# Kernel optimization log

Hardware: AMD Instinct MI355X
Metric: run time of the kernel (lower is better)

Reference implementation:

```python
import jax, jax.numpy as jnp
import numpy as np

N_NODES = 100000


def gcn_conv(x, W, b, src, dst, ew, n):
    """PyG GCNConv with edge_weight: add self-loops (weight 1), symmetric norm,
    linear transform, scatter-add aggregation, bias."""
    h = x @ W                                   # [N, F_out]
    # degree includes the self-loop weight of 1 per node
    deg = jnp.zeros((n,), dtype=x.dtype).at[dst].add(ew) + 1.0
    dinv = jax.lax.rsqrt(deg)                   # deg > 0 always (self-loop)
    norm = dinv[src] * ew * dinv[dst]           # [E]
    agg = jax.ops.segment_sum(h[src] * norm[:, None], dst, num_segments=n)
    # self-loop contribution: norm_ii = dinv[i]^2 * 1
    agg = agg + h * (dinv * dinv)[:, None]
    return agg + b


def setup_inputs() -> dict:
    key = jax.random.key(0)
    ks = jax.random.split(key, 9)
    N, E, F_in, F_h, F_out = N_NODES, 1600000, 128, 64, 10
    x = jax.random.normal(ks[0], (N, F_in), dtype=jnp.float32)
    edge_index = jax.random.randint(ks[1], (2, E), 0, N, dtype=jnp.int64)
    edge_weight = jax.random.uniform(ks[2], (E,), dtype=jnp.float32)
    def glorot(k, fi, fo):
        s = jnp.sqrt(6.0 / (fi + fo))
        return jax.random.uniform(k, (fi, fo), minval=-s, maxval=s, dtype=jnp.float32)
    return {
        "x": x,
        "edge_index": edge_index,
        "edge_weight": edge_weight,
        "W1": glorot(ks[3], F_in, F_h), "b1": jnp.zeros((F_h,), jnp.float32),
        "W2": glorot(ks[4], F_h, F_h), "b2": jnp.zeros((F_h,), jnp.float32),
        "Wfc": glorot(ks[5], F_h, F_out), "bfc": jnp.zeros((F_out,), jnp.float32),
    }


def reference(x, edge_index, edge_weight, W1, b1, W2, b2, Wfc, bfc):
    n = x.shape[0]
    src, dst = edge_index[0], edge_index[1]
    h = gcn_conv(x, W1, b1, src, dst, edge_weight, n)
    h = jax.nn.relu(h)
    h = gcn_conv(h, W2, b2, src, dst, edge_weight, n)
    h = jax.nn.relu(h)
    return h @ Wfc + bfc
```

## Files before the change

kernel.cpp:

```cpp
#include <hip/hip_runtime.h>

static constexpr int F_IN  = 128;
static constexpr int F_H   = 64;
static constexpr int F_OUT = 10;

static constexpr int NPB_SHIFT = 9;
static constexpr int NPB = 1 << NPB_SHIFT;
static constexpr int MAXC = 256;
static constexpr int EPB = 4096;

__device__ __forceinline__ unsigned short f2bf(float f) {
    unsigned u = __float_as_uint(f);
    return (unsigned short)((u + 0x7fff + ((u >> 16) & 1)) >> 16);
}
__device__ __forceinline__ float bf_lo(unsigned u) { return __uint_as_float(u << 16); }
__device__ __forceinline__ float bf_hi(unsigned u) { return __uint_as_float(u & 0xffff0000u); }

__device__ __forceinline__ int load_idx(const void* ein, bool f64, long i) {
    return f64 ? (int)((const long long*)ein)[i] : ((const int*)ein)[i];
}

__global__ __launch_bounds__(256) void k_part1(const void* __restrict__ ein,
                                               const float* __restrict__ ew,
                                               int* __restrict__ gcur,
                                               unsigned long long* __restrict__ packed,
                                               int E, int NC, int cap) {
    __shared__ int lcnt[MAXC];
    __shared__ int lofs[MAXC];
    __shared__ int sflag;
    int tid = threadIdx.x;
    if (tid < NC) lcnt[tid] = 0;
    if (tid < 64) {
        unsigned long long v = ((const unsigned long long*)ein)[tid];
        int hz = ((v >> 32) == 0ull) ? 1 : 0;
        int all64 = __all(hz);
        if (tid == 0) sflag = all64;
    }
    __syncthreads();
    bool f = sflag != 0;
    int base = blockIdx.x * EPB;
    int   es[16];
    int   ed[16];
    float ww[16];
#pragma unroll
    for (int j = 0; j < 16; ++j) {
        int e = base + j * 256 + tid;
        if (e < E) {
            es[j] = load_idx(ein, f, e);
            ed[j] = load_idx(ein, f, (long)E + e);
            ww[j] = ew[e];
            atomicAdd(&lcnt[ed[j] >> NPB_SHIFT], 1);
        }
    }
    __syncthreads();
    if (tid < NC) {
        int c = lcnt[tid];
        lofs[tid] = c ? atomicAdd(&gcur[tid], c) : 0;
        lcnt[tid] = 0;
    }
    __syncthreads();
#pragma unroll
    for (int j = 0; j < 16; ++j) {
        int e = base + j * 256 + tid;
        if (e < E) {
            int b = ed[j] >> NPB_SHIFT;
            int pos = lofs[b] + atomicAdd(&lcnt[b], 1);
            if (pos < cap) {
                unsigned long long u = (unsigned long long)__float_as_uint(ww[j])
                                     | ((unsigned long long)(unsigned)es[j] << 32)
                                     | ((unsigned long long)(unsigned)(ed[j] & (NPB - 1)) << 49);
                packed[(long)b * cap + pos] = u;
            }
        }
    }
}

__global__ __launch_bounds__(256) void k_chist(const unsigned long long* __restrict__ packed,
                                               const int* __restrict__ gcur,
                                               int* __restrict__ rp,
                                               int* __restrict__ pbt,
                                               float* __restrict__ dinv,
                                               int N, int cap) {
    __shared__ int   lc[NPB];
    __shared__ float ld[NPB];
    __shared__ int   sm[256];
    int b = blockIdx.x, tid = threadIdx.x;
#pragma unroll
    for (int i = tid; i < NPB; i += 256) { lc[i] = 0; ld[i] = 0.0f; }
    __syncthreads();
    int cnt = gcur[b];
    const unsigned long long* pk = packed + (long)b * cap;
    for (int p = tid; p < cnt; p += 256) {
        unsigned long long u = pk[p];
        int dl = (int)(u >> 49);
        atomicAdd(&lc[dl], 1);
        atomicAdd(&ld[dl], __uint_as_float((unsigned int)u));
    }
    __syncthreads();
    int c0 = lc[tid * 2], c1 = lc[tid * 2 + 1];
    int pp0 = (c0 + 15) & ~15, pp1 = (c1 + 15) & ~15;
    int s = pp0 + pp1;
    sm[tid] = s;
    __syncthreads();
    for (int off = 1; off < 256; off <<= 1) {
        int v = 0;
        if (tid >= off) v = sm[tid - off];
        __syncthreads();
        sm[tid] += v;
        __syncthreads();
    }
    int excl = sm[tid] - s;
    int n0 = b << NPB_SHIFT;
    int node0 = n0 + tid * 2, node1 = node0 + 1;
    if (node0 < N) {
        rp[node0]   = excl;
        dinv[node0] = rsqrtf(ld[tid * 2] + 1.0f);
    }
    if (node1 < N) {
        rp[node1]   = excl + pp0;
        dinv[node1] = rsqrtf(ld[tid * 2 + 1] + 1.0f);
    }
    if (tid == 255) pbt[b] = sm[255];
}

__global__ __launch_bounds__(256) void k_cscatter(const unsigned long long* __restrict__ packed,
                                                  const int* __restrict__ gcur,
                                                  const int* __restrict__ rp,
                                                  const int* __restrict__ pbt,
                                                  const float* __restrict__ dinv,
                                                  uint2* __restrict__ recs,
                                                  int* __restrict__ rpabs,
                                                  int N, int NC, int cap) {
    __shared__ int   cur[NPB];
    __shared__ float dd[NPB];
    __shared__ int   sm[256];
    int b = blockIdx.x, tid = threadIdx.x;
    int c = (tid < NC) ? pbt[tid] : 0;
    sm[tid] = c;
    __syncthreads();
    for (int off = 1; off < 256; off <<= 1) {
        int v = 0;
        if (tid >= off) v = sm[tid - off];
        __syncthreads();
        sm[tid] += v;
        __syncthreads();
    }
    int pbtb = pbt[b];
    int pb_  = sm[b] - pbtb;
    if (b == NC - 1 && tid == 255) rpabs[N] = sm[255];
    int n0 = b << NPB_SHIFT;
#pragma unroll
    for (int i = tid; i < NPB; i += 256) {
        int node = n0 + i;
        int r = (node < N) ? rp[node] + pb_ : 0;
        cur[i] = r;
        dd[i]  = (node < N) ? dinv[node] : 0.0f;
        if (node < N) rpabs[node] = r;
    }
    __syncthreads();
    int cnt = gcur[b];
    const unsigned long long* pk = packed + (long)b * cap;
    for (int p = tid; p < cnt; p += 256) {
        unsigned long long u = pk[p];
        int dl = (int)(u >> 49);
        int s  = (int)((u >> 32) & 0x1FFFF);
        float w = __uint_as_float((unsigned int)u);
        int pos = atomicAdd(&cur[dl], 1);
        uint2 r;
        r.x = (unsigned)(s << 7);
        r.y = __float_as_uint(dinv[s] * w * dd[dl]);
        recs[pos] = r;
    }
    __syncthreads();
    for (int i = tid; i < NPB; i += 256) {
        int node = n0 + i;
        if (node < N) {
            int el = (i == NPB - 1 || node + 1 >= N) ? pbtb : rp[node + 1];
            int end = el + pb_;
            for (int p = cur[i]; p < end; ++p) recs[p] = make_uint2(0u, 0u);
        }
    }
}

template <int K, bool ABF16>
__global__ __launch_bounds__(256) void k_gemm(const void* __restrict__ A,
                                              const float* __restrict__ W,
                                              unsigned short* __restrict__ Cb, int M) {
    __shared__ float As[128][32];
    __shared__ float Ws[32][64];
    int tid = threadIdx.x;
    int tx = tid & 15;
    int ty = tid >> 4;
    int rb = blockIdx.x * 128;
    float acc[8][4] = {};
    for (int kc = 0; kc < K; kc += 32) {
        __syncthreads();
#pragma unroll
        for (int i = 0; i < 4; ++i) {
            int e = tid + i * 256;
            int r = e >> 3, g = e & 7;
            int gr = rb + r;
            float4 v = make_float4(0.f, 0.f, 0.f, 0.f);
            if (gr < M) {
                if (ABF16) {
                    uint2 u = *(const uint2*)&((const unsigned short*)A)[(long)gr * K + kc + g * 4];
                    v = make_float4(bf_lo(u.x), bf_hi(u.x), bf_lo(u.y), bf_hi(u.y));
                } else {
                    v = *(const float4*)&((const float*)A)[(long)gr * K + kc + g * 4];
                }
            }
            int gs = g ^ ((r >> 3) & 7);
            *(float4*)&As[r][gs * 4] = v;
        }
#pragma unroll
        for (int i = 0; i < 2; ++i) {
            int e = tid + i * 256;
            int k = e >> 4, n4 = e & 15;
            *(float4*)&Ws[k][n4 * 4] = *(const float4*)&W[(long)(kc + k) * 64 + n4 * 4];
        }
        __syncthreads();
#pragma unroll
        for (int g = 0; g < 8; ++g) {
            float4 b0 = *(const float4*)&Ws[g * 4 + 0][tx * 4];
            float4 b1 = *(const float4*)&Ws[g * 4 + 1][tx * 4];
            float4 b2 = *(const float4*)&Ws[g * 4 + 2][tx * 4];
            float4 b3 = *(const float4*)&Ws[g * 4 + 3][tx * 4];
            int gs = (g ^ (ty & 7)) * 4;
#pragma unroll
            for (int rr = 0; rr < 8; ++rr) {
                float4 a = *(const float4*)&As[ty * 8 + rr][gs];
                acc[rr][0] = fmaf(a.x, b0.x, acc[rr][0]);
                acc[rr][1] = fmaf(a.x, b0.y, acc[rr][1]);
                acc[rr][2] = fmaf(a.x, b0.z, acc[rr][2]);
                acc[rr][3] = fmaf(a.x, b0.w, acc[rr][3]);
                acc[rr][0] = fmaf(a.y, b1.x, acc[rr][0]);
                acc[rr][1] = fmaf(a.y, b1.y, acc[rr][1]);
                acc[rr][2] = fmaf(a.y, b1.z, acc[rr][2]);
                acc[rr][3] = fmaf(a.y, b1.w, acc[rr][3]);
                acc[rr][0] = fmaf(a.z, b2.x, acc[rr][0]);
                acc[rr][1] = fmaf(a.z, b2.y, acc[rr][1]);
                acc[rr][2] = fmaf(a.z, b2.z, acc[rr][2]);
                acc[rr][3] = fmaf(a.z, b2.w, acc[rr][3]);
                acc[rr][0] = fmaf(a.w, b3.x, acc[rr][0]);
                acc[rr][1] = fmaf(a.w, b3.y, acc[rr][1]);
                acc[rr][2] = fmaf(a.w, b3.z, acc[rr][2]);
                acc[rr][3] = fmaf(a.w, b3.w, acc[rr][3]);
            }
        }
    }
#pragma unroll
    for (int rr = 0; rr < 8; ++rr) {
        int gr = rb + ty * 8 + rr;
        if (gr < M) {
            ushort4 v;
            v.x = f2bf(acc[rr][0]); v.y = f2bf(acc[rr][1]);
            v.z = f2bf(acc[rr][2]); v.w = f2bf(acc[rr][3]);
            *(ushort4*)&Cb[(long)gr * 64 + tx * 4] = v;
        }
    }
}

__global__ __launch_bounds__(256, 4) void k_agg(const unsigned short* __restrict__ hb,
                                                const int* __restrict__ rp,
                                                const uint2* __restrict__ recs,
                                                const float* __restrict__ dinv,
                                                const float* __restrict__ bias,
                                                unsigned short* __restrict__ outb, int N) {
    int wid  = (blockIdx.x * 256 + threadIdx.x) >> 6;
    int lane = threadIdx.x & 63;
    int fg   = lane & 15;
    int es   = lane >> 4;
    if (wid >= N) return;
    int fg8 = fg * 8;
    const char* hbase = (const char*)hb;
    int p0 = rp[wid], p1 = rp[wid + 1];
    float a0 = 0.f, a1 = 0.f, a2 = 0.f, a3 = 0.f;
    int pb = p0 + es * 4;
    for (; pb + 16 < p1; pb += 32) {
        uint4 r01 = *(const uint4*)&recs[pb];
        uint4 r23 = *(const uint4*)&recs[pb + 2];
        uint4 r45 = *(const uint4*)&recs[pb + 16];
        uint4 r67 = *(const uint4*)&recs[pb + 18];
        uint2 h0 = *(const uint2*)(hbase + r01.x + fg8);
        uint2 h1 = *(const uint2*)(hbase + r01.z + fg8);
        uint2 h2 = *(const uint2*)(hbase + r23.x + fg8);
        uint2 h3 = *(const uint2*)(hbase + r23.z + fg8);
        uint2 h4 = *(const uint2*)(hbase + r45.x + fg8);
        uint2 h5 = *(const uint2*)(hbase + r45.z + fg8);
        uint2 h6 = *(const uint2*)(hbase + r67.x + fg8);
        uint2 h7 = *(const uint2*)(hbase + r67.z + fg8);
        float w0 = __uint_as_float(r01.y), w1 = __uint_as_float(r01.w);
        float w2 = __uint_as_float(r23.y), w3 = __uint_as_float(r23.w);
        float w4 = __uint_as_float(r45.y), w5 = __uint_as_float(r45.w);
        float w6 = __uint_as_float(r67.y), w7 = __uint_as_float(r67.w);
        a0 = fmaf(w0, bf_lo(h0.x), a0); a1 = fmaf(w0, bf_hi(h0.x), a1);
        a2 = fmaf(w0, bf_lo(h0.y), a2); a3 = fmaf(w0, bf_hi(h0.y), a3);
        a0 = fmaf(w1, bf_lo(h1.x), a0); a1 = fmaf(w1, bf_hi(h1.x), a1);
        a2 = fmaf(w1, bf_lo(h1.y), a2); a3 = fmaf(w1, bf_hi(h1.y), a3);
        a0 = fmaf(w2, bf_lo(h2.x), a0); a1 = fmaf(w2, bf_hi(h2.x), a1);
        a2 = fmaf(w2, bf_lo(h2.y), a2); a3 = fmaf(w2, bf_hi(h2.y), a3);
        a0 = fmaf(w3, bf_lo(h3.x), a0); a1 = fmaf(w3, bf_hi(h3.x), a1);
        a2 = fmaf(w3, bf_lo(h3.y), a2); a3 = fmaf(w3, bf_hi(h3.y), a3);
        a0 = fmaf(w4, bf_lo(h4.x), a0); a1 = fmaf(w4, bf_hi(h4.x), a1);
        a2 = fmaf(w4, bf_lo(h4.y), a2); a3 = fmaf(w4, bf_hi(h4.y), a3);
        a0 = fmaf(w5, bf_lo(h5.x), a0); a1 = fmaf(w5, bf_hi(h5.x), a1);
        a2 = fmaf(w5, bf_lo(h5.y), a2); a3 = fmaf(w5, bf_hi(h5.y), a3);
        a0 = fmaf(w6, bf_lo(h6.x), a0); a1 = fmaf(w6, bf_hi(h6.x), a1);
        a2 = fmaf(w6, bf_lo(h6.y), a2); a3 = fmaf(w6, bf_hi(h6.y), a3);
        a0 = fmaf(w7, bf_lo(h7.x), a0); a1 = fmaf(w7, bf_hi(h7.x), a1);
        a2 = fmaf(w7, bf_lo(h7.y), a2); a3 = fmaf(w7, bf_hi(h7.y), a3);
    }
    if (pb < p1) {
        uint4 r01 = *(const uint4*)&recs[pb];
        uint4 r23 = *(const uint4*)&recs[pb + 2];
        uint2 h0 = *(const uint2*)(hbase + r01.x + fg8);
        uint2 h1 = *(const uint2*)(hbase + r01.z + fg8);
        uint2 h2 = *(const uint2*)(hbase + r23.x + fg8);
        uint2 h3 = *(const uint2*)(hbase + r23.z + fg8);
        float w0 = __uint_as_float(r01.y), w1 = __uint_as_float(r01.w);
        float w2 = __uint_as_float(r23.y), w3 = __uint_as_float(r23.w);
        a0 = fmaf(w0, bf_lo(h0.x), a0); a1 = fmaf(w0, bf_hi(h0.x), a1);
        a2 = fmaf(w0, bf_lo(h0.y), a2); a3 = fmaf(w0, bf_hi(h0.y), a3);
        a0 = fmaf(w1, bf_lo(h1.x), a0); a1 = fmaf(w1, bf_hi(h1.x), a1);
        a2 = fmaf(w1, bf_lo(h1.y), a2); a3 = fmaf(w1, bf_hi(h1.y), a3);
        a0 = fmaf(w2, bf_lo(h2.x), a0); a1 = fmaf(w2, bf_hi(h2.x), a1);
        a2 = fmaf(w2, bf_lo(h2.y), a2); a3 = fmaf(w2, bf_hi(h2.y), a3);
        a0 = fmaf(w3, bf_lo(h3.x), a0); a1 = fmaf(w3, bf_hi(h3.x), a1);
        a2 = fmaf(w3, bf_lo(h3.y), a2); a3 = fmaf(w3, bf_hi(h3.y), a3);
    }
#pragma unroll
    for (int m = 16; m <= 32; m <<= 1) {
        a0 += __shfl_xor(a0, m);
        a1 += __shfl_xor(a1, m);
        a2 += __shfl_xor(a2, m);
        a3 += __shfl_xor(a3, m);
    }
    float di  = dinv[wid];
    float di2 = di * di;
    uint2 hs = *(const uint2*)(hbase + ((long)wid << 7) + fg8);
    float4 bv = *(const float4*)&bias[fg * 4];
    a0 = fmaf(bf_lo(hs.x), di2, a0 + bv.x);
    a1 = fmaf(bf_hi(hs.x), di2, a1 + bv.y);
    a2 = fmaf(bf_lo(hs.y), di2, a2 + bv.z);
    a3 = fmaf(bf_hi(hs.y), di2, a3 + bv.w);
    if (es == 0) {
        ushort4 r;
        r.x = f2bf(fmaxf(a0, 0.f));
        r.y = f2bf(fmaxf(a1, 0.f));
        r.z = f2bf(fmaxf(a2, 0.f));
        r.w = f2bf(fmaxf(a3, 0.f));
        *(ushort4*)&outb[(long)wid * 64 + fg * 4] = r;
    }
}

__global__ __launch_bounds__(256) void k_fc(const unsigned short* __restrict__ hb,
                                            const float* __restrict__ W,
                                            const float* __restrict__ b,
                                            float* __restrict__ out, int N) {
    __shared__ float Ws[64 * 10];
    __shared__ float bs[16];
    int tid = threadIdx.x;
    for (int e = tid; e < 64 * 10; e += 256) Ws[e] = W[e];
    if (tid < 10) bs[tid] = b[tid];
    __syncthreads();
    int i = blockIdx.x * 256 + tid;
    if (i >= N) return;
    float acc[10];
#pragma unroll
    for (int j = 0; j < 10; ++j) acc[j] = bs[j];
    const uint2* row = (const uint2*)&hb[(long)i * 64];
#pragma unroll
    for (int c = 0; c < 16; ++c) {
        uint2 u = row[c];
        float ax = bf_lo(u.x), ay = bf_hi(u.x);
        float az = bf_lo(u.y), aw = bf_hi(u.y);
#pragma unroll
        for (int j = 0; j < 10; ++j) {
            acc[j] = fmaf(ax, Ws[(4 * c + 0) * 10 + j], acc[j]);
            acc[j] = fmaf(ay, Ws[(4 * c + 1) * 10 + j], acc[j]);
            acc[j] = fmaf(az, Ws[(4 * c + 2) * 10 + j], acc[j]);
            acc[j] = fmaf(aw, Ws[(4 * c + 3) * 10 + j], acc[j]);
        }
    }
#pragma unroll
    for (int j = 0; j < 10; ++j) out[(long)i * 10 + j] = acc[j];
}

extern "C" void kernel_launch(void* const* d_in, const int* in_sizes, int n_in,
                              void* d_out, int out_size, void* d_ws, size_t ws_size,
                              hipStream_t stream) {
    const float* x    = (const float*)d_in[0];
    const void*  eidx = d_in[1];
    const float* ew   = (const float*)d_in[2];
    const float* W1   = (const float*)d_in[3];
    const float* b1   = (const float*)d_in[4];
    const float* W2   = (const float*)d_in[5];
    const float* b2   = (const float*)d_in[6];
    const float* Wfc  = (const float*)d_in[7];
    const float* bfc  = (const float*)d_in[8];
    float* out = (float*)d_out;

    const int N  = in_sizes[0] / F_IN;
    const int E  = in_sizes[2];
    const int NC = (N + NPB - 1) >> NPB_SHIFT;
    const int cap = E / NC + E / (8 * NC) + 1024;

    char* w = (char*)d_ws;
    size_t off = 0;
    auto alloc = [&](size_t bytes) {
        void* p = w + off;
        off += (bytes + 255) & ~(size_t)255;
        return p;
    };
    float* dinv  = (float*)alloc((size_t)N * 4);
    int*   rp    = (int*)alloc((size_t)(N + 1) * 4);
    int*   rpabs = (int*)alloc((size_t)(N + 1) * 4);
    int*   gcur  = (int*)alloc((size_t)MAXC * 4);
    int*   pbt   = (int*)alloc((size_t)MAXC * 4);
    unsigned long long* packed =
        (unsigned long long*)alloc((size_t)NC * cap * 8);
    uint2* recs  = (uint2*)alloc(((size_t)E + 15u * (size_t)N + 64) * 8);
    unsigned short* h1b = (unsigned short*)alloc((size_t)N * F_H * 2);
    unsigned short* g1b = (unsigned short*)alloc((size_t)N * F_H * 2);
    unsigned short* h2b = h1b;
    unsigned short* g2b = g1b;
    (void)ws_size;

    hipMemsetAsync(gcur, 0, (size_t)NC * 4, stream);

    const int PB = (E + EPB - 1) / EPB;

    k_part1<<<PB, 256, 0, stream>>>(eidx, ew, gcur, packed, E, NC, cap);
    k_chist<<<NC, 256, 0, stream>>>(packed, gcur, rp, pbt, dinv, N, cap);
    k_cscatter<<<NC, 256, 0, stream>>>(packed, gcur, rp, pbt, dinv, recs,
                                       rpabs, N, NC, cap);

    const int GB = (N + 127) / 128;
    k_gemm<F_IN, false><<<GB, 256, 0, stream>>>(x, W1, h1b, N);
    k_agg<<<(N + 3) / 4, 256, 0, stream>>>(h1b, rpabs, recs, dinv, b1, g1b, N);
    k_gemm<F_H, true><<<GB, 256, 0, stream>>>(g1b, W2, h2b, N);
    k_agg<<<(N + 3) / 4, 256, 0, stream>>>(h2b, rpabs, recs, dinv, b2, g2b, N);
    k_fc<<<(N + 255) / 256, 256, 0, stream>>>(g2b, Wfc, bfc, out, N);
}
```

Measured before the change: 203.7 us.

## Merge edge partitioning and first-layer GEMM into one heterogeneous launch

The edge bucketing kernel and the first x@W1 GEMM are combined into a single launch. Blocks below PB do the edge partitioning and the remaining blocks compute the bf16 h1 tiles, so the two independent phases can share the GPU at the same time and one launch is removed. The cost is higher shared memory per block, since the GEMM tiles are always allocated, which may lower occupancy for the partition blocks.

Result: faster. 194.7 us (-4.4%).

```diff
diff --git a/kernel.cpp b/kernel.cpp
--- a/kernel.cpp
+++ b/kernel.cpp
@@ -20,56 +20,127 @@
     return f64 ? (int)((const long long*)ein)[i] : ((const int*)ein)[i];
 }
 
-__global__ __launch_bounds__(256) void k_part1(const void* __restrict__ ein,
-                                               const float* __restrict__ ew,
-                                               int* __restrict__ gcur,
-                                               unsigned long long* __restrict__ packed,
-                                               int E, int NC, int cap) {
+__global__ __launch_bounds__(256) void k_pre(const void* __restrict__ ein,
+                                             const float* __restrict__ ew,
+                                             int* __restrict__ gcur,
+                                             unsigned long long* __restrict__ packed,
+                                             int E, int NC, int cap, int PB,
+                                             const float* __restrict__ x,
+                                             const float* __restrict__ W1,
+                                             unsigned short* __restrict__ h1b, int M) {
     __shared__ int lcnt[MAXC];
     __shared__ int lofs[MAXC];
     __shared__ int sflag;
+    __shared__ float As[128][32];
+    __shared__ float Ws[32][64];
     int tid = threadIdx.x;
-    if (tid < NC) lcnt[tid] = 0;
-    if (tid < 64) {
-        unsigned long long v = ((const unsigned long long*)ein)[tid];
-        int hz = ((v >> 32) == 0ull) ? 1 : 0;
-        int all64 = __all(hz);
-        if (tid == 0) sflag = all64;
-    }
-    __syncthreads();
-    bool f = sflag != 0;
-    int base = blockIdx.x * EPB;
-    int   es[16];
-    int   ed[16];
-    float ww[16];
-#pragma unroll
-    for (int j = 0; j < 16; ++j) {
-        int e = base + j * 256 + tid;
-        if (e < E) {
-            es[j] = load_idx(ein, f, e);
-            ed[j] = load_idx(ein, f, (long)E + e);
-            ww[j] = ew[e];
-            atomicAdd(&lcnt[ed[j] >> NPB_SHIFT], 1);
-        }
-    }
-    __syncthreads();
-    if (tid < NC) {
-        int c = lcnt[tid];
-        lofs[tid] = c ? atomicAdd(&gcur[tid], c) : 0;
-        lcnt[tid] = 0;
-    }
-    __syncthreads();
-#pragma unroll
-    for (int j = 0; j < 16; ++j) {
-        int e = base + j * 256 + tid;
-        if (e < E) {
-            int b = ed[j] >> NPB_SHIFT;
-            int pos = lofs[b] + atomicAdd(&lcnt[b], 1);
-            if (pos < cap) {
-                unsigned long long u = (unsigned long long)__float_as_uint(ww[j])
-                                     | ((unsigned long long)(unsigned)es[j] << 32)
-                                     | ((unsigned long long)(unsigned)(ed[j] & (NPB - 1)) << 49);
-                packed[(long)b * cap + pos] = u;
+    if ((int)blockIdx.x < PB) {
+        if (tid < NC) lcnt[tid] = 0;
+        if (tid < 64) {
+            unsigned long long v = ((const unsigned long long*)ein)[tid];
+            int hz = ((v >> 32) == 0ull) ? 1 : 0;
+            int all64 = __all(hz);
+            if (tid == 0) sflag = all64;
+        }
+        __syncthreads();
+        bool f = sflag != 0;
+        int base = blockIdx.x * EPB;
+        int   es[16];
+        int   ed[16];
+        float ww[16];
+#pragma unroll
+        for (int j = 0; j < 16; ++j) {
+            int e = base + j * 256 + tid;
+            if (e < E) {
+                es[j] = load_idx(ein, f, e);
+                ed[j] = load_idx(ein, f, (long)E + e);
+                ww[j] = ew[e];
+                atomicAdd(&lcnt[ed[j] >> NPB_SHIFT], 1);
+            }
+        }
+        __syncthreads();
+        if (tid < NC) {
+            int c = lcnt[tid];
+            lofs[tid] = c ? atomicAdd(&gcur[tid], c) : 0;
+            lcnt[tid] = 0;
+        }
+        __syncthreads();
+#pragma unroll
+        for (int j = 0; j < 16; ++j) {
+            int e = base + j * 256 + tid;
+            if (e < E) {
+                int b = ed[j] >> NPB_SHIFT;
+                int pos = lofs[b] + atomicAdd(&lcnt[b], 1);
+                if (pos < cap) {
+                    unsigned long long u = (unsigned long long)__float_as_uint(ww[j])
+                                         | ((unsigned long long)(unsigned)es[j] << 32)
+                                         | ((unsigned long long)(unsigned)(ed[j] & (NPB - 1)) << 49);
+                    packed[(long)b * cap + pos] = u;
+                }
+            }
+        }
+    } else {
+        constexpr int K = F_IN;
+        int tx = tid & 15;
+        int ty = tid >> 4;
+        int rb = ((int)blockIdx.x - PB) * 128;
+        float acc[8][4] = {};
+        for (int kc = 0; kc < K; kc += 32) {
+            __syncthreads();
+#pragma unroll
+            for (int i = 0; i < 4; ++i) {
+                int e = tid + i * 256;
+                int r = e >> 3, g = e & 7;
+                int gr = rb + r;
+                float4 v = make_float4(0.f, 0.f, 0.f, 0.f);
+                if (gr < M) v = *(const float4*)&x[(long)gr * K + kc + g * 4];
+                int gs = g ^ ((r >> 3) & 7);
+                *(float4*)&As[r][gs * 4] = v;
+            }
+#pragma unroll
+            for (int i = 0; i < 2; ++i) {
+                int e = tid + i * 256;
+                int k = e >> 4, n4 = e & 15;
+                *(float4*)&Ws[k][n4 * 4] = *(const float4*)&W1[(long)(kc + k) * 64 + n4 * 4];
+            }
+            __syncthreads();
+#pragma unroll
+            for (int g = 0; g < 8; ++g) {
+                float4 b0 = *(const float4*)&Ws[g * 4 + 0][tx * 4];
+                float4 b1 = *(const float4*)&Ws[g * 4 + 1][tx * 4];
+                float4 b2 = *(const float4*)&Ws[g * 4 + 2][tx * 4];
+                float4 b3 = *(const float4*)&Ws[g * 4 + 3][tx * 4];
+                int gs = (g ^ (ty & 7)) * 4;
+#pragma unroll
+                for (int rr = 0; rr < 8; ++rr) {
+                    float4 a = *(const float4*)&As[ty * 8 + rr][gs];
+                    acc[rr][0] = fmaf(a.x, b0.x, acc[rr][0]);
+                    acc[rr][1] = fmaf(a.x, b0.y, acc[rr][1]);
+                    acc[rr][2] = fmaf(a.x, b0.z, acc[rr][2]);
+                    acc[rr][3] = fmaf(a.x, b0.w, acc[rr][3]);
+                    acc[rr][0] = fmaf(a.y, b1.x, acc[rr][0]);
+                    acc[rr][1] = fmaf(a.y, b1.y, acc[rr][1]);
+                    acc[rr][2] = fmaf(a.y, b1.z, acc[rr][2]);
+                    acc[rr][3] = fmaf(a.y, b1.w, acc[rr][3]);
+                    acc[rr][0] = fmaf(a.z, b2.x, acc[rr][0]);
+                    acc[rr][1] = fmaf(a.z, b2.y, acc[rr][1]);
+                    acc[rr][2] = fmaf(a.z, b2.z, acc[rr][2]);
+                    acc[rr][3] = fmaf(a.z, b2.w, acc[rr][3]);
+                    acc[rr][0] = fmaf(a.w, b3.x, acc[rr][0]);
+                    acc[rr][1] = fmaf(a.w, b3.y, acc[rr][1]);
+                    acc[rr][2] = fmaf(a.w, b3.z, acc[rr][2]);
+                    acc[rr][3] = fmaf(a.w, b3.w, acc[rr][3]);
+                }
+            }
+        }
+#pragma unroll
+        for (int rr = 0; rr < 8; ++rr) {
+            int gr = rb + ty * 8 + rr;
+            if (gr < M) {
+                ushort4 v;
+                v.x = f2bf(acc[rr][0]); v.y = f2bf(acc[rr][1]);
+                v.z = f2bf(acc[rr][2]); v.w = f2bf(acc[rr][3]);
+                *(ushort4*)&h1b[(long)gr * 64 + tx * 4] = v;
             }
         }
     }
@@ -429,14 +500,14 @@
     hipMemsetAsync(gcur, 0, (size_t)NC * 4, stream);
 
     const int PB = (E + EPB - 1) / EPB;
-
-    k_part1<<<PB, 256, 0, stream>>>(eidx, ew, gcur, packed, E, NC, cap);
+    const int GB = (N + 127) / 128;
+
+    k_pre<<<PB + GB, 256, 0, stream>>>(eidx, ew, gcur, packed, E, NC, cap, PB,
+                                       x, W1, h1b, N);
     k_chist<<<NC, 256, 0, stream>>>(packed, gcur, rp, pbt, dinv, N, cap);
     k_cscatter<<<NC, 256, 0, stream>>>(packed, gcur, rp, pbt, dinv, recs,
                                        rpabs, N, NC, cap);
 
-    const int GB = (N + 127) / 128;
-    k_gemm<F_IN, false><<<GB, 256, 0, stream>>>(x, W1, h1b, N);
     k_agg<<<(N + 3) / 4, 256, 0, stream>>>(h1b, rpabs, recs, dinv, b1, g1b, N);
     k_gemm<F_H, true><<<GB, 256, 0, stream>>>(g1b, W2, h2b, N);
     k_agg<<<(N + 3) / 4, 256, 0, stream>>>(h2b, rpabs, recs, dinv, b2, g2b, N);
```
